# Kernel optimization log

Hardware: AMD Instinct MI355X
Metric: run time of the kernel (lower is better)

## Reference

```python
import jax, jax.numpy as jnp
import numpy as np

DIM = 16
HID = 128
B = 1024
STEPS = 10  # RK4 steps in differentiable_forward


def setup_inputs() -> dict:
    key = jax.random.key(0)
    ks = jax.random.split(key, 8)

    def lin(k, fan_in, fan_out):
        return jax.random.normal(k, (fan_in, fan_out), jnp.float32) / np.float32(np.sqrt(fan_in))

    W0 = lin(ks[0], DIM + 1, HID)
    W1 = lin(ks[1], HID, HID)
    W2 = lin(ks[2], HID, HID)
    W3 = lin(ks[3], HID, HID)
    W4 = lin(ks[4], HID, DIM)
    b0 = jnp.zeros((HID,), jnp.float32)
    b1 = jnp.zeros((HID,), jnp.float32)
    b2 = jnp.zeros((HID,), jnp.float32)
    b3 = jnp.zeros((HID,), jnp.float32)
    b4 = jnp.zeros((DIM,), jnp.float32)
    x = jax.random.normal(ks[5], (B, DIM), jnp.float32)
    x_star = jax.random.normal(ks[6], (B, DIM), jnp.float32)
    return dict(x=x, x_star=x_star, W0=W0, b0=b0, W1=W1, b1=b1,
                W2=W2, b2=b2, W3=W3, b3=b3, W4=W4, b4=b4)


def reference(x, x_star, W0, b0, W1, b1, W2, b2, W3, b3, W4, b4):
    dtype = x.dtype

    def vel(t, z):
        # z: [..., DIM]; append scalar time channel -> [..., DIM+1]
        tcol = jnp.full(z.shape[:-1] + (1,), t, dtype)
        h = jnp.concatenate([z, tcol], axis=-1)
        h = jnp.tanh(h @ W0 + b0)
        h = jnp.tanh(h @ W1 + b1)
        h = jnp.tanh(h @ W2 + b2)
        h = jnp.tanh(h @ W3 + b3)
        return h @ W4 + b4

    def flow(z):
        # RK4 integration of the velocity field from t=0 to t=1 (10 steps)
        dt = 1.0 / STEPS
        for i in range(STEPS):
            t = i * dt
            k1 = vel(t, z)
            k2 = vel(t + 0.5 * dt, z + 0.5 * dt * k1)
            k3 = vel(t + 0.5 * dt, z + 0.5 * dt * k2)
            k4 = vel(t + dt, z + dt * k3)
            z = z + (k1 + 2.0 * k2 + 2.0 * k3 + k4) * (dt / 6.0)
        return z

    n = x.shape[0]
    y_comb = flow(jnp.concatenate([x, x_star], axis=0))
    y, y_star = y_comb[:n], y_comb[n:]

    diff = y - y_star
    norm = jnp.linalg.norm(diff, axis=1, keepdims=True) + 1e-8
    grad_phi_y = diff / norm  # [B, DIM]

    # Per-sample Jacobian J[b, i, j] = d y_i / d x_j (flow is pointwise per row)
    J = jax.vmap(jax.jacfwd(flow))(x)  # [B, DIM, DIM]

    G = jnp.einsum('bij,bik->bjk', J, J)  # J^T J
    G_inv = jnp.linalg.inv(G + 1e-6 * jnp.eye(DIM, dtype=dtype))
    grad_phi_x = jnp.einsum('bij,bi->bj', J, grad_phi_y)  # J^T grad_phi_y
    x_dot = -jnp.einsum('bjk,bk->bj', G_inv, grad_phi_x)
    return x_dot
```

## Files before the change

### kernel.cpp

```cpp
#include <hip/hip_runtime.h>
#include <math.h>

typedef _Float16 half8  __attribute__((ext_vector_type(8)));
typedef _Float16 half4  __attribute__((ext_vector_type(4)));
typedef float    float4v __attribute__((ext_vector_type(4)));

#define NDIM   16
#define HID    128
#define NSTEP  10
#define RPW    2
#define NROWS  48
#define XSTR   136
#define XISTR  40
#define SBS    17

__device__ __forceinline__ float tanh_fast(float v) {
  float e = __expf(2.f * v);
  return 1.f - 2.f * __builtin_amdgcn_rcpf(e + 1.f);
}

template<int CTRL>
__device__ __forceinline__ float qbcast(float v) {
  int i = __builtin_amdgcn_update_dpp(0, __builtin_bit_cast(int, v), CTRL, 0xF, 0xF, true);
  return __builtin_bit_cast(float, i);
}

__device__ __forceinline__ int oneuron(int c) {
  return 32*(c >> 5) + 16*((c >> 2) & 1) + 4*((c >> 3) & 3) + (c & 3);
}

__global__ __launch_bounds__(256, 2)
void flow_ode_kernel(const float* __restrict__ gx,  const float* __restrict__ gxs,
                     const float* __restrict__ W0,  const float* __restrict__ b0,
                     const float* __restrict__ W1,  const float* __restrict__ b1,
                     const float* __restrict__ W2,  const float* __restrict__ b2,
                     const float* __restrict__ W3,  const float* __restrict__ b3,
                     const float* __restrict__ W4,  const float* __restrict__ b4,
                     float* __restrict__ out)
{
  __shared__ __align__(16) _Float16 XT[2][NROWS][XSTR];
  __shared__ __align__(16) _Float16 XI[NROWS][XISTR];
  __shared__ float SbL[NROWS][SBS];

  const int tid  = threadIdx.x;
  const int mi   = tid >> 6;
  const int lane = tid & 63;
  const int q    = lane >> 4;
  const int ln   = lane & 15;
  const int g0   = blockIdx.x * RPW;

  half8 A0[2];
  half8 A1[2][4], A2[2][4], A3[2][4];
  half8 A4[4];
  float bw[4][2][4];
  float b4r[4];

  #pragma unroll
  for (int mt = 0; mt < 2; ++mt) {
    const int m = 16*(2*mi + mt) + ln;
    #pragma unroll
    for (int j = 0; j < 8; ++j) {
      const int k = 8*q + j;
      A0[mt][j] = (k < NDIM+1) ? (_Float16)W0[k*HID + m] : (_Float16)0.f;
    }
    #pragma unroll
    for (int ks = 0; ks < 4; ++ks) {
      #pragma unroll
      for (int j = 0; j < 8; ++j) {
        const int k = oneuron(32*ks + 8*q + j);
        A1[mt][ks][j] = (_Float16)W1[k*HID + m];
        A2[mt][ks][j] = (_Float16)W2[k*HID + m];
        A3[mt][ks][j] = (_Float16)W3[k*HID + m];
      }
    }
  }
  #pragma unroll
  for (int ks = 0; ks < 4; ++ks)
    #pragma unroll
    for (int j = 0; j < 8; ++j)
      A4[ks][j] = (_Float16)W4[oneuron(32*ks + 8*q + j)*NDIM + ln];

  #pragma unroll
  for (int mt = 0; mt < 2; ++mt)
    #pragma unroll
    for (int r = 0; r < 4; ++r) {
      const int m = 16*(2*mi + mt) + 4*q + r;
      bw[0][mt][r] = b0[m];
      bw[1][mt][r] = b1[m];
      bw[2][mt][r] = b2[m];
      bw[3][mt][r] = b3[m];
    }
  #pragma unroll
  for (int r = 0; r < 4; ++r) b4r[r] = b4[4*q + r];

  float sbr[4], sar[4];
  if (mi == 0) {
    const int p = ln & 3;
    const float* src = (p < 2) ? (gx + (g0 + p)*NDIM) : (gxs + (g0 + p - 2)*NDIM);
    #pragma unroll
    for (int r = 0; r < 4; ++r) sbr[r] = src[4*q + r];
  } else {
    #pragma unroll
    for (int r = 0; r < 4; ++r) sbr[r] = (ln == 4*q + r) ? 1.f : 0.f;
  }
  #pragma unroll
  for (int r = 0; r < 4; ++r) sar[r] = 0.f;

  for (int idx = tid; idx < NROWS*32; idx += 256)
    XI[idx >> 5][idx & 31] = (_Float16)0.f;
  __syncthreads();
  if (mi < 3) {
    half4 x4;
    #pragma unroll
    for (int r = 0; r < 4; ++r) x4[r] = (_Float16)sbr[r];
    *(half4*)&XI[mi*16 + ln][4*q] = x4;
  }
  __syncthreads();

  if (blockIdx.x & 1) __builtin_amdgcn_s_sleep(22);

  const float dt = 1.f / NSTEP;

  auto finish = [&](float4v (&D)[2][3], int wb) {
    float ss[2][4];
    half8 hh;
    #pragma unroll
    for (int mt = 0; mt < 2; ++mt)
      #pragma unroll
      for (int r = 0; r < 4; ++r) {
        const float h = tanh_fast(D[mt][0][r]);
        hh[4*mt + r] = (_Float16)h;
        ss[mt][r] = 1.f - h*h;
      }
    *(half8*)&XT[wb][ln][32*mi + 8*q] = hh;
    half8 t1, t2;
    #pragma unroll
    for (int mt = 0; mt < 2; ++mt)
      #pragma unroll
      for (int r = 0; r < 4; ++r) {
        t1[4*mt + r] = (_Float16)(D[mt][1][r] * qbcast<0x00>(ss[mt][r]));
        t2[4*mt + r] = (_Float16)(D[mt][2][r] * qbcast<0x55>(ss[mt][r]));
      }
    *(half8*)&XT[wb][16 + ln][32*mi + 8*q] = t1;
    *(half8*)&XT[wb][32 + ln][32*mi + 8*q] = t2;
    __syncthreads();
  };

  auto mid_layer = [&](const half8 (&A)[2][4], const float (&bb)[2][4], int rb, int wb) {
    float4v D[2][3];
    #pragma unroll
    for (int mt = 0; mt < 2; ++mt)
      #pragma unroll
      for (int nt = 0; nt < 3; ++nt)
        #pragma unroll
        for (int e = 0; e < 4; ++e) D[mt][nt][e] = (nt == 0) ? bb[mt][e] : 0.f;
    #pragma unroll
    for (int ks = 0; ks < 4; ++ks) {
      half8 Bf[3];
      #pragma unroll
      for (int nt = 0; nt < 3; ++nt)
        Bf[nt] = *(const half8*)&XT[rb][nt*16 + ln][32*ks + 8*q];
      #pragma unroll
      for (int nt = 0; nt < 3; ++nt) {
        D[0][nt] = __builtin_amdgcn_mfma_f32_16x16x32_f16(A[0][ks], Bf[nt], D[0][nt], 0, 0, 0);
        D[1][nt] = __builtin_amdgcn_mfma_f32_16x16x32_f16(A[1][ks], Bf[nt], D[1][nt], 0, 0, 0);
      }
    }
    finish(D, wb);
  };

  #pragma unroll 1
  for (int step = 0; step < NSTEP; ++step) {
    const float t0 = step * dt;
    #pragma unroll
    for (int stage = 0; stage < 4; ++stage) {
      {
        float4v D[2][3];
        #pragma unroll
        for (int mt = 0; mt < 2; ++mt)
          #pragma unroll
          for (int nt = 0; nt < 3; ++nt)
            #pragma unroll
            for (int e = 0; e < 4; ++e) D[mt][nt][e] = (nt == 0) ? bw[0][mt][e] : 0.f;
        half8 Bf[3];
        #pragma unroll
        for (int nt = 0; nt < 3; ++nt)
          Bf[nt] = *(const half8*)&XI[nt*16 + ln][8*q];
        #pragma unroll
        for (int nt = 0; nt < 3; ++nt) {
          D[0][nt] = __builtin_amdgcn_mfma_f32_16x16x32_f16(A0[0], Bf[nt], D[0][nt], 0, 0, 0);
          D[1][nt] = __builtin_amdgcn_mfma_f32_16x16x32_f16(A0[1], Bf[nt], D[1][nt], 0, 0, 0);
        }
        finish(D, 0);
      }
      mid_layer(A1, bw[1], 0, 1);
      mid_layer(A2, bw[2], 1, 0);
      mid_layer(A3, bw[3], 0, 1);
      {
        if (mi < 3) {
          float4v Da;
          #pragma unroll
          for (int e = 0; e < 4; ++e) Da[e] = (mi == 0) ? b4r[e] : 0.f;
          #pragma unroll
          for (int ks = 0; ks < 4; ++ks) {
            half8 Ba = *(const half8*)&XT[1][mi*16 + ln][32*ks + 8*q];
            Da = __builtin_amdgcn_mfma_f32_16x16x32_f16(A4[ks], Ba, Da, 0, 0, 0);
          }
          const float c_s = (stage < 2) ? 0.5f*dt : dt;
          half4 xn;
          if (stage < 3) {
            const float w_s = (stage == 0) ? 1.f : 2.f;
            #pragma unroll
            for (int r = 0; r < 4; ++r) {
              sar[r] += w_s * Da[r];
              xn[r] = (_Float16)(sbr[r] + c_s * Da[r]);
            }
          } else {
            #pragma unroll
            for (int r = 0; r < 4; ++r) {
              const float nb = sbr[r] + (dt * (1.f/6.f)) * (sar[r] + Da[r]);
              sbr[r] = nb;
              sar[r] = 0.f;
              xn[r] = (_Float16)nb;
            }
          }
          *(half4*)&XI[mi*16 + ln][4*q] = xn;
          if (mi == 0 && q == 0)
            XI[ln][16] = (_Float16)(t0 + ((stage < 2) ? 0.5f*dt : dt));
        }
        __syncthreads();
      }
    }
  }

  if (mi < 3) {
    #pragma unroll
    for (int r = 0; r < 4; ++r)
      SbL[mi*16 + ln][4*q + r] = sbr[r];
  }
  __syncthreads();

  if (mi < RPW) {
    const int p    = mi;
    const int jj   = ln;
    const int base = lane & 48;
    float c[NDIM], gv[NDIM], G[NDIM];
    #pragma unroll
    for (int i = 0; i < NDIM; ++i) c[i] = SbL[16 + 16*p + jj][i];
    float n2 = 0.f;
    #pragma unroll
    for (int i = 0; i < NDIM; ++i) {
      gv[i] = SbL[p][i] - SbL[2 + p][i];
      n2 += gv[i]*gv[i];
    }
    const float rinv = 1.f / (sqrtf(n2) + 1e-8f);
    float rhs = 0.f;
    #pragma unroll
    for (int i = 0; i < NDIM; ++i) rhs += c[i] * gv[i];
    rhs *= rinv;
    #pragma unroll
    for (int k = 0; k < NDIM; ++k) {
      float acc = (k == jj) ? 1e-6f : 0.f;
      #pragma unroll
      for (int i = 0; i < NDIM; ++i)
        acc += c[i] * __shfl(c[i], base + k, 64);
      G[k] = acc;
    }
    #pragma unroll
    for (int k = 0; k < NDIM-1; ++k) {
      const float piv  = __shfl(G[k], base + k, 64);
      const float prhs = __shfl(rhs,  base + k, 64);
      const float f = (jj > k) ? G[k] / piv : 0.f;
      #pragma unroll
      for (int cc = k; cc < NDIM; ++cc)
        G[cc] -= f * __shfl(G[cc], base + k, 64);
      rhs -= f * prhs;
    }
    float sol = 0.f;
    #pragma unroll
    for (int k = NDIM-1; k >= 0; --k) {
      const float piv = __shfl(G[k], base + k, 64);
      const float pr  = __shfl(rhs,  base + k, 64);
      const float xk  = pr / piv;
      if (jj == k) sol = xk;
      if (jj <  k) rhs -= G[k] * xk;
    }
    if (lane < NDIM)
      out[(g0 + p)*NDIM + jj] = -sol;
  }
}

extern "C" void kernel_launch(void* const* d_in, const int* in_sizes, int n_in,
                              void* d_out, int out_size, void* d_ws, size_t ws_size,
                              hipStream_t stream) {
  (void)in_sizes; (void)n_in; (void)d_ws; (void)ws_size; (void)out_size;
  flow_ode_kernel<<<dim3(512), dim3(256), 0, stream>>>(
      (const float*)d_in[0],  (const float*)d_in[1],
      (const float*)d_in[2],  (const float*)d_in[3],
      (const float*)d_in[4],  (const float*)d_in[5],
      (const float*)d_in[6],  (const float*)d_in[7],
      (const float*)d_in[8],  (const float*)d_in[9],
      (const float*)d_in[10], (const float*)d_in[11],
      (float*)d_out);
}
```

Before: 237.0 us.

## Process two independent sample groups per block with interleaved MFMA chains

```diff
diff --git a/kernel.cpp b/kernel.cpp
--- a/kernel.cpp
+++ b/kernel.cpp
@@ -8,7 +8,7 @@
 #define NDIM   16
 #define HID    128
 #define NSTEP  10
-#define RPW    2
+#define RPW    4
 #define NROWS  48
 #define XSTR   136
 #define XISTR  40
@@ -29,7 +29,7 @@
   return 32*(c >> 5) + 16*((c >> 2) & 1) + 4*((c >> 3) & 3) + (c & 3);
 }
 
-__global__ __launch_bounds__(256, 2)
+__global__ __launch_bounds__(256, 1)
 void flow_ode_kernel(const float* __restrict__ gx,  const float* __restrict__ gxs,
                      const float* __restrict__ W0,  const float* __restrict__ b0,
                      const float* __restrict__ W1,  const float* __restrict__ b1,
@@ -38,9 +38,10 @@
                      const float* __restrict__ W4,  const float* __restrict__ b4,
                      float* __restrict__ out)
 {
-  __shared__ __align__(16) _Float16 XT[2][NROWS][XSTR];
-  __shared__ __align__(16) _Float16 XI[NROWS][XISTR];
-  __shared__ float SbL[NROWS][SBS];
+  __shared__ __align__(16) _Float16 XTA[2][NROWS][XSTR];
+  __shared__ __align__(16) _Float16 XTB[2][NROWS][XSTR];
+  __shared__ __align__(16) _Float16 XIA[NROWS][XISTR];
+  __shared__ __align__(16) _Float16 XIB[NROWS][XISTR];
 
   const int tid  = threadIdx.x;
   const int mi   = tid >> 6;
@@ -93,80 +94,117 @@
   #pragma unroll
   for (int r = 0; r < 4; ++r) b4r[r] = b4[4*q + r];
 
-  float sbr[4], sar[4];
+  float sbrA[4], sarA[4], sbrB[4], sarB[4];
   if (mi == 0) {
     const int p = ln & 3;
-    const float* src = (p < 2) ? (gx + (g0 + p)*NDIM) : (gxs + (g0 + p - 2)*NDIM);
-    #pragma unroll
-    for (int r = 0; r < 4; ++r) sbr[r] = src[4*q + r];
+    const float* srcA = (p < 2) ? (gx + (g0 + p)*NDIM)     : (gxs + (g0 + p - 2)*NDIM);
+    const float* srcB = (p < 2) ? (gx + (g0 + 2 + p)*NDIM) : (gxs + (g0 + p)*NDIM);
+    #pragma unroll
+    for (int r = 0; r < 4; ++r) { sbrA[r] = srcA[4*q + r]; sbrB[r] = srcB[4*q + r]; }
   } else {
     #pragma unroll
-    for (int r = 0; r < 4; ++r) sbr[r] = (ln == 4*q + r) ? 1.f : 0.f;
-  }
-  #pragma unroll
-  for (int r = 0; r < 4; ++r) sar[r] = 0.f;
-
-  for (int idx = tid; idx < NROWS*32; idx += 256)
-    XI[idx >> 5][idx & 31] = (_Float16)0.f;
+    for (int r = 0; r < 4; ++r) {
+      const float e = (ln == 4*q + r) ? 1.f : 0.f;
+      sbrA[r] = e; sbrB[r] = e;
+    }
+  }
+  #pragma unroll
+  for (int r = 0; r < 4; ++r) { sarA[r] = 0.f; sarB[r] = 0.f; }
+
+  for (int idx = tid; idx < NROWS*32; idx += 256) {
+    XIA[idx >> 5][idx & 31] = (_Float16)0.f;
+    XIB[idx >> 5][idx & 31] = (_Float16)0.f;
+  }
   __syncthreads();
   if (mi < 3) {
-    half4 x4;
-    #pragma unroll
-    for (int r = 0; r < 4; ++r) x4[r] = (_Float16)sbr[r];
-    *(half4*)&XI[mi*16 + ln][4*q] = x4;
+    half4 xa, xb;
+    #pragma unroll
+    for (int r = 0; r < 4; ++r) { xa[r] = (_Float16)sbrA[r]; xb[r] = (_Float16)sbrB[r]; }
+    *(half4*)&XIA[mi*16 + ln][4*q] = xa;
+    *(half4*)&XIB[mi*16 + ln][4*q] = xb;
   }
   __syncthreads();
 
-  if (blockIdx.x & 1) __builtin_amdgcn_s_sleep(22);
-
   const float dt = 1.f / NSTEP;
 
-  auto finish = [&](float4v (&D)[2][3], int wb) {
-    float ss[2][4];
-    half8 hh;
-    #pragma unroll
-    for (int mt = 0; mt < 2; ++mt)
-      #pragma unroll
-      for (int r = 0; r < 4; ++r) {
-        const float h = tanh_fast(D[mt][0][r]);
-        hh[4*mt + r] = (_Float16)h;
-        ss[mt][r] = 1.f - h*h;
-      }
-    *(half8*)&XT[wb][ln][32*mi + 8*q] = hh;
-    half8 t1, t2;
-    #pragma unroll
-    for (int mt = 0; mt < 2; ++mt)
-      #pragma unroll
-      for (int r = 0; r < 4; ++r) {
-        t1[4*mt + r] = (_Float16)(D[mt][1][r] * qbcast<0x00>(ss[mt][r]));
-        t2[4*mt + r] = (_Float16)(D[mt][2][r] * qbcast<0x55>(ss[mt][r]));
-      }
-    *(half8*)&XT[wb][16 + ln][32*mi + 8*q] = t1;
-    *(half8*)&XT[wb][32 + ln][32*mi + 8*q] = t2;
+  auto finish2 = [&](float4v (&DA)[2][3], float4v (&DB)[2][3], int wb) {
+    {
+      float ss[2][4];
+      half8 hh;
+      #pragma unroll
+      for (int mt = 0; mt < 2; ++mt)
+        #pragma unroll
+        for (int r = 0; r < 4; ++r) {
+          const float h = tanh_fast(DA[mt][0][r]);
+          hh[4*mt + r] = (_Float16)h;
+          ss[mt][r] = 1.f - h*h;
+        }
+      *(half8*)&XTA[wb][ln][32*mi + 8*q] = hh;
+      half8 t1, t2;
+      #pragma unroll
+      for (int mt = 0; mt < 2; ++mt)
+        #pragma unroll
+        for (int r = 0; r < 4; ++r) {
+          t1[4*mt + r] = (_Float16)(DA[mt][1][r] * qbcast<0x00>(ss[mt][r]));
+          t2[4*mt + r] = (_Float16)(DA[mt][2][r] * qbcast<0x55>(ss[mt][r]));
+        }
+      *(half8*)&XTA[wb][16 + ln][32*mi + 8*q] = t1;
+      *(half8*)&XTA[wb][32 + ln][32*mi + 8*q] = t2;
+    }
+    {
+      float ss[2][4];
+      half8 hh;
+      #pragma unroll
+      for (int mt = 0; mt < 2; ++mt)
+        #pragma unroll
+        for (int r = 0; r < 4; ++r) {
+          const float h = tanh_fast(DB[mt][0][r]);
+          hh[4*mt + r] = (_Float16)h;
+          ss[mt][r] = 1.f - h*h;
+        }
+      *(half8*)&XTB[wb][ln][32*mi + 8*q] = hh;
+      half8 t1, t2;
+      #pragma unroll
+      for (int mt = 0; mt < 2; ++mt)
+        #pragma unroll
+        for (int r = 0; r < 4; ++r) {
+          t1[4*mt + r] = (_Float16)(DB[mt][1][r] * qbcast<0x00>(ss[mt][r]));
+          t2[4*mt + r] = (_Float16)(DB[mt][2][r] * qbcast<0x55>(ss[mt][r]));
+        }
+      *(half8*)&XTB[wb][16 + ln][32*mi + 8*q] = t1;
+      *(half8*)&XTB[wb][32 + ln][32*mi + 8*q] = t2;
+    }
     __syncthreads();
   };
 
-  auto mid_layer = [&](const half8 (&A)[2][4], const float (&bb)[2][4], int rb, int wb) {
-    float4v D[2][3];
+  auto mid2 = [&](const half8 (&A)[2][4], const float (&bb)[2][4], int rb, int wb) {
+    float4v DA[2][3], DB[2][3];
     #pragma unroll
     for (int mt = 0; mt < 2; ++mt)
       #pragma unroll
       for (int nt = 0; nt < 3; ++nt)
         #pragma unroll
-        for (int e = 0; e < 4; ++e) D[mt][nt][e] = (nt == 0) ? bb[mt][e] : 0.f;
+        for (int e = 0; e < 4; ++e) {
+          DA[mt][nt][e] = (nt == 0) ? bb[mt][e] : 0.f;
+          DB[mt][nt][e] = (nt == 0) ? bb[mt][e] : 0.f;
+        }
     #pragma unroll
     for (int ks = 0; ks < 4; ++ks) {
-      half8 Bf[3];
-      #pragma unroll
-      for (int nt = 0; nt < 3; ++nt)
-        Bf[nt] = *(const half8*)&XT[rb][nt*16 + ln][32*ks + 8*q];
+      half8 BA[3], BB[3];
       #pragma unroll
       for (int nt = 0; nt < 3; ++nt) {
-        D[0][nt] = __builtin_amdgcn_mfma_f32_16x16x32_f16(A[0][ks], Bf[nt], D[0][nt], 0, 0, 0);
-        D[1][nt] = __builtin_amdgcn_mfma_f32_16x16x32_f16(A[1][ks], Bf[nt], D[1][nt], 0, 0, 0);
-      }
-    }
-    finish(D, wb);
+        BA[nt] = *(const half8*)&XTA[rb][nt*16 + ln][32*ks + 8*q];
+        BB[nt] = *(const half8*)&XTB[rb][nt*16 + ln][32*ks + 8*q];
+      }
+      #pragma unroll
+      for (int nt = 0; nt < 3; ++nt) {
+        DA[0][nt] = __builtin_amdgcn_mfma_f32_16x16x32_f16(A[0][ks], BA[nt], DA[0][nt], 0, 0, 0);
+        DA[1][nt] = __builtin_amdgcn_mfma_f32_16x16x32_f16(A[1][ks], BA[nt], DA[1][nt], 0, 0, 0);
+        DB[0][nt] = __builtin_amdgcn_mfma_f32_16x16x32_f16(A[0][ks], BB[nt], DB[0][nt], 0, 0, 0);
+        DB[1][nt] = __builtin_amdgcn_mfma_f32_16x16x32_f16(A[1][ks], BB[nt], DB[1][nt], 0, 0, 0);
+      }
+    }
+    finish2(DA, DB, wb);
   };
 
   #pragma unroll 1
@@ -175,82 +213,106 @@
     #pragma unroll
     for (int stage = 0; stage < 4; ++stage) {
       {
-        float4v D[2][3];
+        float4v DA[2][3], DB[2][3];
         #pragma unroll
         for (int mt = 0; mt < 2; ++mt)
           #pragma unroll
           for (int nt = 0; nt < 3; ++nt)
             #pragma unroll
-            for (int e = 0; e < 4; ++e) D[mt][nt][e] = (nt == 0) ? bw[0][mt][e] : 0.f;
-        half8 Bf[3];
-        #pragma unroll
-        for (int nt = 0; nt < 3; ++nt)
-          Bf[nt] = *(const half8*)&XI[nt*16 + ln][8*q];
+            for (int e = 0; e < 4; ++e) {
+              DA[mt][nt][e] = (nt == 0) ? bw[0][mt][e] : 0.f;
+              DB[mt][nt][e] = (nt == 0) ? bw[0][mt][e] : 0.f;
+            }
+        half8 BA[3], BB[3];
         #pragma unroll
         for (int nt = 0; nt < 3; ++nt) {
-          D[0][nt] = __builtin_amdgcn_mfma_f32_16x16x32_f16(A0[0], Bf[nt], D[0][nt], 0, 0, 0);
-          D[1][nt] = __builtin_amdgcn_mfma_f32_16x16x32_f16(A0[1], Bf[nt], D[1][nt], 0, 0, 0);
-        }
-        finish(D, 0);
-      }
-      mid_layer(A1, bw[1], 0, 1);
-      mid_layer(A2, bw[2], 1, 0);
-      mid_layer(A3, bw[3], 0, 1);
+          BA[nt] = *(const half8*)&XIA[nt*16 + ln][8*q];
+          BB[nt] = *(const half8*)&XIB[nt*16 + ln][8*q];
+        }
+        #pragma unroll
+        for (int nt = 0; nt < 3; ++nt) {
+          DA[0][nt] = __builtin_amdgcn_mfma_f32_16x16x32_f16(A0[0], BA[nt], DA[0][nt], 0, 0, 0);
+          DA[1][nt] = __builtin_amdgcn_mfma_f32_16x16x32_f16(A0[1], BA[nt], DA[1][nt], 0, 0, 0);
+          DB[0][nt] = __builtin_amdgcn_mfma_f32_16x16x32_f16(A0[0], BB[nt], DB[0][nt], 0, 0, 0);
+          DB[1][nt] = __builtin_amdgcn_mfma_f32_16x16x32_f16(A0[1], BB[nt], DB[1][nt], 0, 0, 0);
+        }
+        finish2(DA, DB, 0);
+      }
+      mid2(A1, bw[1], 0, 1);
+      mid2(A2, bw[2], 1, 0);
+      mid2(A3, bw[3], 0, 1);
       {
         if (mi < 3) {
-          float4v Da;
+          float4v DaA, DaB;
           #pragma unroll
-          for (int e = 0; e < 4; ++e) Da[e] = (mi == 0) ? b4r[e] : 0.f;
+          for (int e = 0; e < 4; ++e) {
+            const float bi = (mi == 0) ? b4r[e] : 0.f;
+            DaA[e] = bi; DaB[e] = bi;
+          }
           #pragma unroll
           for (int ks = 0; ks < 4; ++ks) {
-            half8 Ba = *(const half8*)&XT[1][mi*16 + ln][32*ks + 8*q];
-            Da = __builtin_amdgcn_mfma_f32_16x16x32_f16(A4[ks], Ba, Da, 0, 0, 0);
+            half8 BaA = *(const half8*)&XTA[1][mi*16 + ln][32*ks + 8*q];
+            half8 BaB = *(const half8*)&XTB[1][mi*16 + ln][32*ks + 8*q];
+            DaA = __builtin_amdgcn_mfma_f32_16x16x32_f16(A4[ks], BaA, DaA, 0, 0, 0);
+            DaB = __builtin_amdgcn_mfma_f32_16x16x32_f16(A4[ks], BaB, DaB, 0, 0, 0);
           }
           const float c_s = (stage < 2) ? 0.5f*dt : dt;
-          half4 xn;
+          half4 xnA, xnB;
           if (stage < 3) {
             const float w_s = (stage == 0) ? 1.f : 2.f;
             #pragma unroll
             for (int r = 0; r < 4; ++r) {
-              sar[r] += w_s * Da[r];
-              xn[r] = (_Float16)(sbr[r] + c_s * Da[r]);
+              sarA[r] += w_s * DaA[r];
+              sarB[r] += w_s * DaB[r];
+              xnA[r] = (_Float16)(sbrA[r] + c_s * DaA[r]);
+              xnB[r] = (_Float16)(sbrB[r] + c_s * DaB[r]);
             }
           } else {
             #pragma unroll
             for (int r = 0; r < 4; ++r) {
-              const float nb = sbr[r] + (dt * (1.f/6.f)) * (sar[r] + Da[r]);
-              sbr[r] = nb;
-              sar[r] = 0.f;
-              xn[r] = (_Float16)nb;
+              const float nbA = sbrA[r] + (dt * (1.f/6.f)) * (sarA[r] + DaA[r]);
+              const float nbB = sbrB[r] + (dt * (1.f/6.f)) * (sarB[r] + DaB[r]);
+              sbrA[r] = nbA; sarA[r] = 0.f; xnA[r] = (_Float16)nbA;
+              sbrB[r] = nbB; sarB[r] = 0.f; xnB[r] = (_Float16)nbB;
             }
           }
-          *(half4*)&XI[mi*16 + ln][4*q] = xn;
-          if (mi == 0 && q == 0)
-            XI[ln][16] = (_Float16)(t0 + ((stage < 2) ? 0.5f*dt : dt));
+          *(half4*)&XIA[mi*16 + ln][4*q] = xnA;
+          *(half4*)&XIB[mi*16 + ln][4*q] = xnB;
+          if (mi == 0 && q == 0) {
+            const _Float16 tc = (_Float16)(t0 + ((stage < 2) ? 0.5f*dt : dt));
+            XIA[ln][16] = tc;
+            XIB[ln][16] = tc;
+          }
         }
         __syncthreads();
       }
     }
   }
 
+  float* SbLA = reinterpret_cast<float*>(&XIA[0][0]);
+  float* SbLB = reinterpret_cast<float*>(&XIB[0][0]);
+  __syncthreads();
   if (mi < 3) {
     #pragma unroll
-    for (int r = 0; r < 4; ++r)
-      SbL[mi*16 + ln][4*q + r] = sbr[r];
+    for (int r = 0; r < 4; ++r) {
+      SbLA[(mi*16 + ln)*SBS + 4*q + r] = sbrA[r];
+      SbLB[(mi*16 + ln)*SBS + 4*q + r] = sbrB[r];
+    }
   }
   __syncthreads();
 
-  if (mi < RPW) {
-    const int p    = mi;
+  {
+    const float* Sb = (mi < 2) ? SbLA : SbLB;
+    const int p    = mi & 1;
     const int jj   = ln;
     const int base = lane & 48;
     float c[NDIM], gv[NDIM], G[NDIM];
     #pragma unroll
-    for (int i = 0; i < NDIM; ++i) c[i] = SbL[16 + 16*p + jj][i];
+    for (int i = 0; i < NDIM; ++i) c[i] = Sb[(16 + 16*p + jj)*SBS + i];
     float n2 = 0.f;
     #pragma unroll
     for (int i = 0; i < NDIM; ++i) {
-      gv[i] = SbL[p][i] - SbL[2 + p][i];
+      gv[i] = Sb[p*SBS + i] - Sb[(2 + p)*SBS + i];
       n2 += gv[i]*gv[i];
     }
     const float rinv = 1.f / (sqrtf(n2) + 1e-8f);
@@ -286,7 +348,7 @@
       if (jj <  k) rhs -= G[k] * xk;
     }
     if (lane < NDIM)
-      out[(g0 + p)*NDIM + jj] = -sol;
+      out[(g0 + mi)*NDIM + jj] = -sol;
   }
 }
 
@@ -294,7 +356,7 @@
                               void* d_out, int out_size, void* d_ws, size_t ws_size,
                               hipStream_t stream) {
   (void)in_sizes; (void)n_in; (void)d_ws; (void)ws_size; (void)out_size;
-  flow_ode_kernel<<<dim3(512), dim3(256), 0, stream>>>(
+  flow_ode_kernel<<<dim3(256), dim3(256), 0, stream>>>(
       (const float*)d_in[0],  (const float*)d_in[1],
       (const float*)d_in[2],  (const float*)d_in[3],
       (const float*)d_in[4],  (const float*)d_in[5],
```

Result: slower. 260.4 us (+9.9%).

## Fold output layer into first layer via precomputed W4·W0 product and carried preactivations

Applied to the files above, without the earlier changes.

```diff
diff --git a/kernel.cpp b/kernel.cpp
--- a/kernel.cpp
+++ b/kernel.cpp
@@ -51,9 +51,12 @@
 
   half8 A0[2];
   half8 A1[2][4], A2[2][4], A3[2][4];
+  half8 AM[2][4];
   half8 A4[4];
   float bw[4][2][4];
   float b4r[4];
+  float bcv[2][4];
+  float w0t[2][4];
 
   #pragma unroll
   for (int mt = 0; mt < 2; ++mt) {
@@ -61,7 +64,7 @@
     #pragma unroll
     for (int j = 0; j < 8; ++j) {
       const int k = 8*q + j;
-      A0[mt][j] = (k < NDIM+1) ? (_Float16)W0[k*HID + m] : (_Float16)0.f;
+      A0[mt][j] = (k < NDIM) ? (_Float16)W0[k*HID + m] : (_Float16)0.f;
     }
     #pragma unroll
     for (int ks = 0; ks < 4; ++ks) {
@@ -73,6 +76,19 @@
         A3[mt][ks][j] = (_Float16)W3[k*HID + m];
       }
     }
+    float w0c[NDIM];
+    #pragma unroll
+    for (int i = 0; i < NDIM; ++i) w0c[i] = W0[i*HID + m];
+    #pragma unroll
+    for (int ks = 0; ks < 4; ++ks)
+      #pragma unroll
+      for (int j = 0; j < 8; ++j) {
+        const int k = oneuron(32*ks + 8*q + j);
+        float acc = 0.f;
+        #pragma unroll
+        for (int i = 0; i < NDIM; ++i) acc += W4[k*NDIM + i] * w0c[i];
+        AM[mt][ks][j] = (_Float16)acc;
+      }
   }
   #pragma unroll
   for (int ks = 0; ks < 4; ++ks)
@@ -89,6 +105,11 @@
       bw[1][mt][r] = b1[m];
       bw[2][mt][r] = b2[m];
       bw[3][mt][r] = b3[m];
+      w0t[mt][r] = W0[NDIM*HID + m];
+      float acc = 0.f;
+      #pragma unroll
+      for (int i = 0; i < NDIM; ++i) acc += b4[i] * W0[i*HID + m];
+      bcv[mt][r] = acc;
     }
   #pragma unroll
   for (int r = 0; r < 4; ++r) b4r[r] = b4[4*q + r];
@@ -117,9 +138,33 @@
   }
   __syncthreads();
 
-  if (blockIdx.x & 1) __builtin_amdgcn_s_sleep(22);
-
   const float dt = 1.f / NSTEP;
+
+  float4v U[2][3], UA[2][3];
+
+  auto emit0 = [&](float tn) {
+    float ss[2][4];
+    half8 hh;
+    #pragma unroll
+    for (int mt = 0; mt < 2; ++mt)
+      #pragma unroll
+      for (int r = 0; r < 4; ++r) {
+        const float h = tanh_fast(U[mt][0][r] + bw[0][mt][r] + tn*w0t[mt][r]);
+        hh[4*mt + r] = (_Float16)h;
+        ss[mt][r] = 1.f - h*h;
+      }
+    *(half8*)&XT[0][ln][32*mi + 8*q] = hh;
+    half8 t1, t2;
+    #pragma unroll
+    for (int mt = 0; mt < 2; ++mt)
+      #pragma unroll
+      for (int r = 0; r < 4; ++r) {
+        t1[4*mt + r] = (_Float16)(U[mt][1][r] * qbcast<0x00>(ss[mt][r]));
+        t2[4*mt + r] = (_Float16)(U[mt][2][r] * qbcast<0x55>(ss[mt][r]));
+      }
+    *(half8*)&XT[0][16 + ln][32*mi + 8*q] = t1;
+    *(half8*)&XT[0][32 + ln][32*mi + 8*q] = t2;
+  };
 
   auto finish = [&](float4v (&D)[2][3], int wb) {
     float ss[2][4];
@@ -169,67 +214,136 @@
     finish(D, wb);
   };
 
+  auto comp = [&](int stage, float t0) {
+    float4v D[2][3];
+    #pragma unroll
+    for (int mt = 0; mt < 2; ++mt)
+      #pragma unroll
+      for (int nt = 0; nt < 3; ++nt)
+        #pragma unroll
+        for (int e = 0; e < 4; ++e) D[mt][nt][e] = 0.f;
+    float4v Da;
+    #pragma unroll
+    for (int e = 0; e < 4; ++e) Da[e] = (mi == 0) ? b4r[e] : 0.f;
+    #pragma unroll
+    for (int ks = 0; ks < 4; ++ks) {
+      half8 Bf[3];
+      #pragma unroll
+      for (int nt = 0; nt < 3; ++nt)
+        Bf[nt] = *(const half8*)&XT[1][nt*16 + ln][32*ks + 8*q];
+      #pragma unroll
+      for (int nt = 0; nt < 3; ++nt) {
+        D[0][nt] = __builtin_amdgcn_mfma_f32_16x16x32_f16(AM[0][ks], Bf[nt], D[0][nt], 0, 0, 0);
+        D[1][nt] = __builtin_amdgcn_mfma_f32_16x16x32_f16(AM[1][ks], Bf[nt], D[1][nt], 0, 0, 0);
+      }
+      if (mi < 3) {
+        half8 Ba = *(const half8*)&XT[1][mi*16 + ln][32*ks + 8*q];
+        Da = __builtin_amdgcn_mfma_f32_16x16x32_f16(A4[ks], Ba, Da, 0, 0, 0);
+      }
+    }
+    const float c_s = (stage < 2) ? 0.5f*dt : dt;
+    const float tn  = t0 + c_s;
+    if (stage < 3) {
+      const float w_s = (stage == 0) ? 1.f : 2.f;
+      #pragma unroll
+      for (int mt = 0; mt < 2; ++mt)
+        #pragma unroll
+        for (int nt = 0; nt < 3; ++nt)
+          #pragma unroll
+          for (int e = 0; e < 4; ++e) UA[mt][nt][e] += w_s * D[mt][nt][e];
+      if (mi < 3) {
+        #pragma unroll
+        for (int r = 0; r < 4; ++r) sar[r] += w_s * Da[r];
+      }
+      float ss[2][4];
+      half8 hh;
+      #pragma unroll
+      for (int mt = 0; mt < 2; ++mt)
+        #pragma unroll
+        for (int r = 0; r < 4; ++r) {
+          const float h = tanh_fast(U[mt][0][r] + c_s*(D[mt][0][r] + bcv[mt][r])
+                                    + bw[0][mt][r] + tn*w0t[mt][r]);
+          hh[4*mt + r] = (_Float16)h;
+          ss[mt][r] = 1.f - h*h;
+        }
+      *(half8*)&XT[0][ln][32*mi + 8*q] = hh;
+      half8 t1, t2;
+      #pragma unroll
+      for (int mt = 0; mt < 2; ++mt)
+        #pragma unroll
+        for (int r = 0; r < 4; ++r) {
+          t1[4*mt + r] = (_Float16)((U[mt][1][r] + c_s*D[mt][1][r]) * qbcast<0x00>(ss[mt][r]));
+          t2[4*mt + r] = (_Float16)((U[mt][2][r] + c_s*D[mt][2][r]) * qbcast<0x55>(ss[mt][r]));
+        }
+      *(half8*)&XT[0][16 + ln][32*mi + 8*q] = t1;
+      *(half8*)&XT[0][32 + ln][32*mi + 8*q] = t2;
+    } else {
+      #pragma unroll
+      for (int mt = 0; mt < 2; ++mt)
+        #pragma unroll
+        for (int nt = 0; nt < 3; ++nt)
+          #pragma unroll
+          for (int e = 0; e < 4; ++e) {
+            U[mt][nt][e] += (dt * (1.f/6.f)) * (UA[mt][nt][e] + D[mt][nt][e]);
+            UA[mt][nt][e] = 0.f;
+          }
+      #pragma unroll
+      for (int mt = 0; mt < 2; ++mt)
+        #pragma unroll
+        for (int r = 0; r < 4; ++r) U[mt][0][r] += dt * bcv[mt][r];
+      if (mi < 3) {
+        #pragma unroll
+        for (int r = 0; r < 4; ++r) {
+          sbr[r] += (dt * (1.f/6.f)) * (sar[r] + Da[r]);
+          sar[r] = 0.f;
+        }
+      }
+      emit0(tn);
+    }
+    __syncthreads();
+  };
+
+  {
+    float4v D0[2][3];
+    #pragma unroll
+    for (int mt = 0; mt < 2; ++mt)
+      #pragma unroll
+      for (int nt = 0; nt < 3; ++nt)
+        #pragma unroll
+        for (int e = 0; e < 4; ++e) D0[mt][nt][e] = 0.f;
+    half8 Bf[3];
+    #pragma unroll
+    for (int nt = 0; nt < 3; ++nt)
+      Bf[nt] = *(const half8*)&XI[nt*16 + ln][8*q];
+    #pragma unroll
+    for (int nt = 0; nt < 3; ++nt) {
+      D0[0][nt] = __builtin_amdgcn_mfma_f32_16x16x32_f16(A0[0], Bf[nt], D0[0][nt], 0, 0, 0);
+      D0[1][nt] = __builtin_amdgcn_mfma_f32_16x16x32_f16(A0[1], Bf[nt], D0[1][nt], 0, 0, 0);
+    }
+    #pragma unroll
+    for (int mt = 0; mt < 2; ++mt)
+      #pragma unroll
+      for (int nt = 0; nt < 3; ++nt)
+        #pragma unroll
+        for (int e = 0; e < 4; ++e) {
+          U[mt][nt][e]  = D0[mt][nt][e];
+          UA[mt][nt][e] = 0.f;
+        }
+    emit0(0.f);
+    __syncthreads();
+  }
+
+  if (blockIdx.x & 1) __builtin_amdgcn_s_sleep(22);
+
   #pragma unroll 1
   for (int step = 0; step < NSTEP; ++step) {
     const float t0 = step * dt;
     #pragma unroll
     for (int stage = 0; stage < 4; ++stage) {
-      {
-        float4v D[2][3];
-        #pragma unroll
-        for (int mt = 0; mt < 2; ++mt)
-          #pragma unroll
-          for (int nt = 0; nt < 3; ++nt)
-            #pragma unroll
-            for (int e = 0; e < 4; ++e) D[mt][nt][e] = (nt == 0) ? bw[0][mt][e] : 0.f;
-        half8 Bf[3];
-        #pragma unroll
-        for (int nt = 0; nt < 3; ++nt)
-          Bf[nt] = *(const half8*)&XI[nt*16 + ln][8*q];
-        #pragma unroll
-        for (int nt = 0; nt < 3; ++nt) {
-          D[0][nt] = __builtin_amdgcn_mfma_f32_16x16x32_f16(A0[0], Bf[nt], D[0][nt], 0, 0, 0);
-          D[1][nt] = __builtin_amdgcn_mfma_f32_16x16x32_f16(A0[1], Bf[nt], D[1][nt], 0, 0, 0);
-        }
-        finish(D, 0);
-      }
       mid_layer(A1, bw[1], 0, 1);
       mid_layer(A2, bw[2], 1, 0);
       mid_layer(A3, bw[3], 0, 1);
-      {
-        if (mi < 3) {
-          float4v Da;
-          #pragma unroll
-          for (int e = 0; e < 4; ++e) Da[e] = (mi == 0) ? b4r[e] : 0.f;
-          #pragma unroll
-          for (int ks = 0; ks < 4; ++ks) {
-            half8 Ba = *(const half8*)&XT[1][mi*16 + ln][32*ks + 8*q];
-            Da = __builtin_amdgcn_mfma_f32_16x16x32_f16(A4[ks], Ba, Da, 0, 0, 0);
-          }
-          const float c_s = (stage < 2) ? 0.5f*dt : dt;
-          half4 xn;
-          if (stage < 3) {
-            const float w_s = (stage == 0) ? 1.f : 2.f;
-            #pragma unroll
-            for (int r = 0; r < 4; ++r) {
-              sar[r] += w_s * Da[r];
-              xn[r] = (_Float16)(sbr[r] + c_s * Da[r]);
-            }
-          } else {
-            #pragma unroll
-            for (int r = 0; r < 4; ++r) {
-              const float nb = sbr[r] + (dt * (1.f/6.f)) * (sar[r] + Da[r]);
-              sbr[r] = nb;
-              sar[r] = 0.f;
-              xn[r] = (_Float16)nb;
-            }
-          }
-          *(half4*)&XI[mi*16 + ln][4*q] = xn;
-          if (mi == 0 && q == 0)
-            XI[ln][16] = (_Float16)(t0 + ((stage < 2) ? 0.5f*dt : dt));
-        }
-        __syncthreads();
-      }
+      comp(stage, t0);
     }
   }
 
```

Result: slower. 850.9 us (+259.0%).
